# Optimization experiments

Measured on AMD Instinct MI355X. Metric: run time of the kernel, lower is better.

The kernel has to match this reference:

```python
import jax, jax.numpy as jnp
import numpy as np

N = 100000
E = 1000000
D = 32          # numerical_dim
HID = 64        # hidden_dim
OUT = 1         # output_dim
REL = 4 * D     # relation feature dim
EPS = 1e-8


def setup_inputs() -> dict:
    key = jax.random.key(0)
    k_x, k_e, k_w1, k_b1, k_w2, k_b2 = jax.random.split(key, 6)
    x = jax.random.uniform(k_x, (N, D), dtype=jnp.float32)
    edge_index = jax.random.randint(k_e, (2, E), 0, N, dtype=jnp.int64)
    # Linear params (PyTorch convention: W [out, in], y = x @ W.T + b)
    lim1 = 1.0 / np.sqrt(REL)
    W1 = jax.random.uniform(k_w1, (HID, REL), minval=-lim1, maxval=lim1, dtype=jnp.float32)
    b1 = jax.random.uniform(k_b1, (HID,), minval=-lim1, maxval=lim1, dtype=jnp.float32)
    lim2 = 1.0 / np.sqrt(HID)
    W2 = jax.random.uniform(k_w2, (OUT, HID), minval=-lim2, maxval=lim2, dtype=jnp.float32)
    b2 = jax.random.uniform(k_b2, (OUT,), minval=-lim2, maxval=lim2, dtype=jnp.float32)
    return {"x": x, "edge_index": edge_index, "W1": W1, "b1": b1, "W2": W2, "b2": b2}


def _relation_features(x_i, x_j):
    ratio = x_i / (x_j + EPS)
    log_ratio = jnp.log(x_i + EPS) - jnp.log(x_j + EPS)
    abs_diff = jnp.abs(x_i - x_j)
    rel_diff = abs_diff / (jnp.maximum(x_i, x_j) + EPS)
    return jnp.concatenate([ratio, log_ratio, abs_diff, rel_diff], axis=-1)  # [E, 4D]


def reference(x, edge_index, W1, b1, W2, b2):
    src, dst = edge_index[0], edge_index[1]
    x_i = x[src]                      # [E, D] gather source node feats
    x_j = x[dst]                      # [E, D] gather target node feats
    rel = _relation_features(x_i, x_j)  # [E, 4D]
    h = jax.nn.relu(rel @ W1.T + b1)    # [E, HID]
    edge_bias = (h @ W2.T + b2).squeeze(-1)  # [E]
    return edge_bias
```

## Files before the change

kernel.cpp:

```cpp
#include <hip/hip_runtime.h>


#define DD    32
#define HID   64
#define RELF  128
#define EPSF  1e-8f

typedef short  bf16x8 __attribute__((ext_vector_type(8)));
typedef float  f32x4  __attribute__((ext_vector_type(4)));

union U8 { unsigned u[4]; bf16x8 v; };

static __device__ __forceinline__ unsigned pk_tr(float lo, float hi) {
    return __builtin_amdgcn_perm(__builtin_bit_cast(unsigned, hi),
                                 __builtin_bit_cast(unsigned, lo), 0x07060302u);
}
static __device__ __forceinline__ unsigned rne_bits(float f) {
    unsigned u = __builtin_bit_cast(unsigned, f);
    return u + 0x7fffu + ((u >> 16) & 1u);
}
static __device__ __forceinline__ unsigned pk_rne(float lo, float hi) {
    return __builtin_amdgcn_perm(rne_bits(hi), rne_bits(lo), 0x07060302u);
}
static __device__ __forceinline__ float hi_f32(float f) {
    return __builtin_bit_cast(float, __builtin_bit_cast(unsigned, f) & 0xffff0000u);
}

__global__ __launch_bounds__(256)
void prep_logx(const float* __restrict__ x, unsigned* __restrict__ lx, int nq)
{
    int i = blockIdx.x * blockDim.x + threadIdx.x;
    if (i >= nq) return;
    float4 v = ((const float4*)x)[i];
    uint2 o;
    o.x = pk_rne(__logf(v.x + EPSF), __logf(v.y + EPSF));
    o.y = pk_rne(__logf(v.z + EPSF), __logf(v.w + EPSF));
    ((uint2*)lx)[i] = o;
}

template <int PRE>
__global__ __launch_bounds__(256, 2)
void edge_bias_mfma(const float* __restrict__ x,
                    const int*   __restrict__ ei,
                    const float* __restrict__ W1,
                    const float* __restrict__ b1,
                    const float* __restrict__ W2,
                    const float* __restrict__ b2,
                    const short* __restrict__ lx,
                    float* __restrict__ out,
                    int E)
{
    const int lane = threadIdx.x & 63;
    const int wave = (blockIdx.x * blockDim.x + threadIdx.x) >> 6;
    const int nwv  = (gridDim.x * blockDim.x) >> 6;
    const int c = lane & 15;
    const int q = lane >> 4;

    bf16x8 W0h[4], W0l[4], WL[4], WLn[4], WA[4], WDm[4];
    #pragma unroll
    for (int nt = 0; nt < 4; ++nt) {
        const float* wr = W1 + (nt * 16 + c) * RELF + q * 8;
        U8 h, l, t;
        #pragma unroll
        for (int p = 0; p < 4; ++p) {
            float w0 = wr[2 * p], w1 = wr[2 * p + 1];
            h.u[p] = pk_tr(w0, w1);
            l.u[p] = pk_rne(w0 - hi_f32(w0), w1 - hi_f32(w1));
        }
        W0h[nt] = h.v; W0l[nt] = l.v;
        #pragma unroll
        for (int p = 0; p < 4; ++p)
            t.u[p] = pk_rne(wr[32 + 2 * p], wr[32 + 2 * p + 1]);
        WL[nt] = t.v;
        #pragma unroll
        for (int p = 0; p < 4; ++p) t.u[p] ^= 0x80008000u;
        WLn[nt] = t.v;
        #pragma unroll
        for (int p = 0; p < 4; ++p)
            t.u[p] = pk_rne(wr[64 + 2 * p], wr[64 + 2 * p + 1]);
        WA[nt] = t.v;
        #pragma unroll
        for (int p = 0; p < 4; ++p)
            t.u[p] = pk_rne(wr[96 + 2 * p], wr[96 + 2 * p + 1]);
        WDm[nt] = t.v;
    }
    float b1v[4], w2v[4];
    #pragma unroll
    for (int nt = 0; nt < 4; ++nt) {
        b1v[nt] = b1[nt * 16 + c];
        w2v[nt] = W2[nt * 16 + c];
    }
    const float b2s = b2[0];

    const int ntiles = (E + 15) >> 4;
    for (int t = wave; t < ntiles; t += nwv) {
        const int e0 = t << 4;
        int em = e0 + c; if (em > E - 1) em = E - 1;
        const int src = ei[em];
        const int dst = ei[E + em];

        const float* pxi = x + (long)src * DD + q * 8;
        const float* pxj = x + (long)dst * DD + q * 8;
        float4 xi0 = ((const float4*)pxi)[0], xi1 = ((const float4*)pxi)[1];
        float4 xj0 = ((const float4*)pxj)[0], xj1 = ((const float4*)pxj)[1];
        float xiv[8] = {xi0.x, xi0.y, xi0.z, xi0.w, xi1.x, xi1.y, xi1.z, xi1.w};
        float xjv[8] = {xj0.x, xj0.y, xj0.z, xj0.w, xj1.x, xj1.y, xj1.z, xj1.w};

        bf16x8 aLi, aLj;
        if constexpr (PRE) {
            aLi = *(const bf16x8*)(lx + (long)src * DD + q * 8);
            aLj = *(const bf16x8*)(lx + (long)dst * DD + q * 8);
        } else {
            U8 ti, tj;
            #pragma unroll
            for (int p = 0; p < 4; ++p) {
                ti.u[p] = pk_rne(__logf(xiv[2*p] + EPSF), __logf(xiv[2*p+1] + EPSF));
                tj.u[p] = pk_rne(__logf(xjv[2*p] + EPSF), __logf(xjv[2*p+1] + EPSF));
            }
            aLi = ti.v; aLj = tj.v;
        }

        U8 R, Rl, Aa, Dd;
        #pragma unroll
        for (int p = 0; p < 4; ++p) {
            float a0 = xiv[2*p], a1 = xiv[2*p+1];
            float c0 = xjv[2*p], c1 = xjv[2*p+1];
            float r0 = a0 * __builtin_amdgcn_rcpf(c0 + EPSF);
            float r1 = a1 * __builtin_amdgcn_rcpf(c1 + EPSF);
            float d0 = fabsf(a0 - c0), d1 = fabsf(a1 - c1);
            float g0 = d0 * __builtin_amdgcn_rcpf(fmaxf(a0, c0) + EPSF);
            float g1 = d1 * __builtin_amdgcn_rcpf(fmaxf(a1, c1) + EPSF);
            R.u[p]  = pk_tr(r0, r1);
            Rl.u[p] = pk_tr(r0 - hi_f32(r0), r1 - hi_f32(r1));
            Aa.u[p] = pk_tr(d0, d1);
            Dd.u[p] = pk_tr(g0, g1);
        }

        f32x4 acc[4];
        #pragma unroll
        for (int nt = 0; nt < 4; ++nt) {
            acc[nt][0] = b1v[nt]; acc[nt][1] = b1v[nt];
            acc[nt][2] = b1v[nt]; acc[nt][3] = b1v[nt];
        }
        #pragma unroll
        for (int nt = 0; nt < 4; ++nt) {
            acc[nt] = __builtin_amdgcn_mfma_f32_16x16x32_bf16(R.v,  W0h[nt], acc[nt], 0, 0, 0);
            acc[nt] = __builtin_amdgcn_mfma_f32_16x16x32_bf16(Rl.v, W0h[nt], acc[nt], 0, 0, 0);
            acc[nt] = __builtin_amdgcn_mfma_f32_16x16x32_bf16(R.v,  W0l[nt], acc[nt], 0, 0, 0);
            acc[nt] = __builtin_amdgcn_mfma_f32_16x16x32_bf16(aLi,  WL[nt],  acc[nt], 0, 0, 0);
            acc[nt] = __builtin_amdgcn_mfma_f32_16x16x32_bf16(aLj,  WLn[nt], acc[nt], 0, 0, 0);
            acc[nt] = __builtin_amdgcn_mfma_f32_16x16x32_bf16(Aa.v, WA[nt],  acc[nt], 0, 0, 0);
            acc[nt] = __builtin_amdgcn_mfma_f32_16x16x32_bf16(Dd.v, WDm[nt], acc[nt], 0, 0, 0);
        }

        float p[4];
        #pragma unroll
        for (int r = 0; r < 4; ++r) {
            float pp = 0.f;
            #pragma unroll
            for (int nt = 0; nt < 4; ++nt)
                pp = fmaf(fmaxf(acc[nt][r], 0.f), w2v[nt], pp);
            pp += __shfl_xor(pp, 1);
            pp += __shfl_xor(pp, 2);
            pp += __shfl_xor(pp, 4);
            pp += __shfl_xor(pp, 8);
            p[r] = pp;
        }
        if (c < 4) {
            const int e = e0 + q * 4 + c;
            if (e < E) {
                float v = (c == 0) ? p[0] : (c == 1) ? p[1] : (c == 2) ? p[2] : p[3];
                out[e] = v + b2s;
            }
        }
    }
}

extern "C" void kernel_launch(void* const* d_in, const int* in_sizes, int n_in,
                              void* d_out, int out_size, void* d_ws, size_t ws_size,
                              hipStream_t stream)
{
    const float* x   = (const float*)d_in[0];
    const int*   ei  = (const int*)  d_in[1];
    const float* W1  = (const float*)d_in[2];
    const float* b1  = (const float*)d_in[3];
    const float* W2  = (const float*)d_in[4];
    const float* b2  = (const float*)d_in[5];
    float* out = (float*)d_out;

    const int E  = out_size;
    const int Nd = in_sizes[0];
    short* lx = (short*)d_ws;

    const bool pre = ws_size >= (size_t)Nd * sizeof(short) && (Nd % 4) == 0;
    if (pre) {
        const int nq = Nd / 4;
        prep_logx<<<(nq + 255) / 256, 256, 0, stream>>>(x, (unsigned*)lx, nq);
        edge_bias_mfma<1><<<1024, 256, 0, stream>>>(x, ei, W1, b1, W2, b2, lx, out, E);
    } else {
        edge_bias_mfma<0><<<1024, 256, 0, stream>>>(x, ei, W1, b1, W2, b2, lx, out, E);
    }
}
```

Measured before the change: 151.2 us.

## Software-pipeline edge index and feature gathers across tile iterations

Restructures the grid-stride loop so each wave prefetches the node features for the next tile and the edge indices for the tile after that while computing the current tile. This is meant to hide the dependent index-then-gather global memory latency behind the MFMA and elementwise work. In exchange it holds more live registers for the prefetched float4 and bf16x8 buffers, which can raise VGPR pressure under launch_bounds(256,2) and issue redundant loads on the final iterations.

```diff
diff --git a/kernel.cpp b/kernel.cpp
--- a/kernel.cpp
+++ b/kernel.cpp
@@ -60,7 +60,7 @@
     #pragma unroll
     for (int nt = 0; nt < 4; ++nt) {
         const float* wr = W1 + (nt * 16 + c) * RELF + q * 8;
-        U8 h, l, t;
+        U8 h, l, tt;
         #pragma unroll
         for (int p = 0; p < 4; ++p) {
             float w0 = wr[2 * p], w1 = wr[2 * p + 1];
@@ -70,19 +70,19 @@
         W0h[nt] = h.v; W0l[nt] = l.v;
         #pragma unroll
         for (int p = 0; p < 4; ++p)
-            t.u[p] = pk_rne(wr[32 + 2 * p], wr[32 + 2 * p + 1]);
-        WL[nt] = t.v;
-        #pragma unroll
-        for (int p = 0; p < 4; ++p) t.u[p] ^= 0x80008000u;
-        WLn[nt] = t.v;
+            tt.u[p] = pk_rne(wr[32 + 2 * p], wr[32 + 2 * p + 1]);
+        WL[nt] = tt.v;
+        #pragma unroll
+        for (int p = 0; p < 4; ++p) tt.u[p] ^= 0x80008000u;
+        WLn[nt] = tt.v;
         #pragma unroll
         for (int p = 0; p < 4; ++p)
-            t.u[p] = pk_rne(wr[64 + 2 * p], wr[64 + 2 * p + 1]);
-        WA[nt] = t.v;
+            tt.u[p] = pk_rne(wr[64 + 2 * p], wr[64 + 2 * p + 1]);
+        WA[nt] = tt.v;
         #pragma unroll
         for (int p = 0; p < 4; ++p)
-            t.u[p] = pk_rne(wr[96 + 2 * p], wr[96 + 2 * p + 1]);
-        WDm[nt] = t.v;
+            tt.u[p] = pk_rne(wr[96 + 2 * p], wr[96 + 2 * p + 1]);
+        WDm[nt] = tt.v;
     }
     float b1v[4], w2v[4];
     #pragma unroll
@@ -93,23 +93,58 @@
     const float b2s = b2[0];
 
     const int ntiles = (E + 15) >> 4;
-    for (int t = wave; t < ntiles; t += nwv) {
+    int t = wave;
+    if (t >= ntiles) return;
+
+    float4 xi0C, xi1C, xj0C, xj1C;
+    bf16x8 LiC, LjC;
+    int srcN, dstN;
+
+    {
+        int em = (t << 4) + c; if (em > E - 1) em = E - 1;
+        int s = ei[em], d = ei[E + em];
+        const float* pi = x + (long)s * DD + q * 8;
+        const float* pj = x + (long)d * DD + q * 8;
+        xi0C = ((const float4*)pi)[0]; xi1C = ((const float4*)pi)[1];
+        xj0C = ((const float4*)pj)[0]; xj1C = ((const float4*)pj)[1];
+        if (PRE) {
+            LiC = *(const bf16x8*)(lx + (long)s * DD + q * 8);
+            LjC = *(const bf16x8*)(lx + (long)d * DD + q * 8);
+        }
+    }
+    {
+        int t1 = t + nwv; if (t1 >= ntiles) t1 = t;
+        int em = (t1 << 4) + c; if (em > E - 1) em = E - 1;
+        srcN = ei[em]; dstN = ei[E + em];
+    }
+
+    for (; t < ntiles; t += nwv) {
+        float4 xi0N, xi1N, xj0N, xj1N;
+        bf16x8 LiN, LjN;
+        {
+            const float* pi = x + (long)srcN * DD + q * 8;
+            const float* pj = x + (long)dstN * DD + q * 8;
+            xi0N = ((const float4*)pi)[0]; xi1N = ((const float4*)pi)[1];
+            xj0N = ((const float4*)pj)[0]; xj1N = ((const float4*)pj)[1];
+            if (PRE) {
+                LiN = *(const bf16x8*)(lx + (long)srcN * DD + q * 8);
+                LjN = *(const bf16x8*)(lx + (long)dstN * DD + q * 8);
+            }
+        }
+        int srcN2, dstN2;
+        {
+            int t2 = t + 2 * nwv; if (t2 >= ntiles) t2 = t;
+            int em = (t2 << 4) + c; if (em > E - 1) em = E - 1;
+            srcN2 = ei[em]; dstN2 = ei[E + em];
+        }
+
         const int e0 = t << 4;
-        int em = e0 + c; if (em > E - 1) em = E - 1;
-        const int src = ei[em];
-        const int dst = ei[E + em];
-
-        const float* pxi = x + (long)src * DD + q * 8;
-        const float* pxj = x + (long)dst * DD + q * 8;
-        float4 xi0 = ((const float4*)pxi)[0], xi1 = ((const float4*)pxi)[1];
-        float4 xj0 = ((const float4*)pxj)[0], xj1 = ((const float4*)pxj)[1];
-        float xiv[8] = {xi0.x, xi0.y, xi0.z, xi0.w, xi1.x, xi1.y, xi1.z, xi1.w};
-        float xjv[8] = {xj0.x, xj0.y, xj0.z, xj0.w, xj1.x, xj1.y, xj1.z, xj1.w};
+        float xiv[8] = {xi0C.x, xi0C.y, xi0C.z, xi0C.w, xi1C.x, xi1C.y, xi1C.z, xi1C.w};
+        float xjv[8] = {xj0C.x, xj0C.y, xj0C.z, xj0C.w, xj1C.x, xj1C.y, xj1C.z, xj1C.w};
 
         bf16x8 aLi, aLj;
         if constexpr (PRE) {
-            aLi = *(const bf16x8*)(lx + (long)src * DD + q * 8);
-            aLj = *(const bf16x8*)(lx + (long)dst * DD + q * 8);
+            aLi = LiC; aLj = LjC;
         } else {
             U8 ti, tj;
             #pragma unroll
@@ -173,6 +208,10 @@
                 out[e] = v + b2s;
             }
         }
+
+        xi0C = xi0N; xi1C = xi1N; xj0C = xj0N; xj1C = xj1N;
+        LiC = LiN;  LjC = LjN;
+        srcN = srcN2; dstN = dstN2;
     }
 }
 
```

After: 144.9 us. -4.2%, faster.

## Software-pipeline edge index loads and feature gathers across tile iterations

Applied to the files above, without the earlier changes.

Restructures the persistent per-wave tile loop into a two-stage double-buffered pipeline. Node features and log features for the next tile are gathered, and edge indices two tiles ahead are loaded, while the current tile's MFMA work runs. The aim is to hide the dependent-index gather latency in a memory-bound kernel, at the cost of more live registers that may press on the 2-blocks-per-CU occupancy target. Out-of-range prefetch tiles are clamped to a valid tile so no loads go out of bounds.

```diff
diff --git a/kernel.cpp b/kernel.cpp
--- a/kernel.cpp
+++ b/kernel.cpp
@@ -60,7 +60,7 @@
     #pragma unroll
     for (int nt = 0; nt < 4; ++nt) {
         const float* wr = W1 + (nt * 16 + c) * RELF + q * 8;
-        U8 h, l, t;
+        U8 h, l, tt;
         #pragma unroll
         for (int p = 0; p < 4; ++p) {
             float w0 = wr[2 * p], w1 = wr[2 * p + 1];
@@ -70,19 +70,19 @@
         W0h[nt] = h.v; W0l[nt] = l.v;
         #pragma unroll
         for (int p = 0; p < 4; ++p)
-            t.u[p] = pk_rne(wr[32 + 2 * p], wr[32 + 2 * p + 1]);
-        WL[nt] = t.v;
-        #pragma unroll
-        for (int p = 0; p < 4; ++p) t.u[p] ^= 0x80008000u;
-        WLn[nt] = t.v;
+            tt.u[p] = pk_rne(wr[32 + 2 * p], wr[32 + 2 * p + 1]);
+        WL[nt] = tt.v;
+        #pragma unroll
+        for (int p = 0; p < 4; ++p) tt.u[p] ^= 0x80008000u;
+        WLn[nt] = tt.v;
         #pragma unroll
         for (int p = 0; p < 4; ++p)
-            t.u[p] = pk_rne(wr[64 + 2 * p], wr[64 + 2 * p + 1]);
-        WA[nt] = t.v;
+            tt.u[p] = pk_rne(wr[64 + 2 * p], wr[64 + 2 * p + 1]);
+        WA[nt] = tt.v;
         #pragma unroll
         for (int p = 0; p < 4; ++p)
-            t.u[p] = pk_rne(wr[96 + 2 * p], wr[96 + 2 * p + 1]);
-        WDm[nt] = t.v;
+            tt.u[p] = pk_rne(wr[96 + 2 * p], wr[96 + 2 * p + 1]);
+        WDm[nt] = tt.v;
     }
     float b1v[4], w2v[4];
     #pragma unroll
@@ -93,24 +93,33 @@
     const float b2s = b2[0];
 
     const int ntiles = (E + 15) >> 4;
-    for (int t = wave; t < ntiles; t += nwv) {
-        const int e0 = t << 4;
-        int em = e0 + c; if (em > E - 1) em = E - 1;
-        const int src = ei[em];
-        const int dst = ei[E + em];
-
-        const float* pxi = x + (long)src * DD + q * 8;
-        const float* pxj = x + (long)dst * DD + q * 8;
-        float4 xi0 = ((const float4*)pxi)[0], xi1 = ((const float4*)pxi)[1];
-        float4 xj0 = ((const float4*)pxj)[0], xj1 = ((const float4*)pxj)[1];
+    int t = wave;
+    if (t >= ntiles) return;
+
+    auto ldidx = [&](int tt, int& s, int& d) {
+        if (tt >= ntiles) tt = t;
+        int em = (tt << 4) + c; if (em > E - 1) em = E - 1;
+        s = ei[em]; d = ei[E + em];
+    };
+    auto gather = [&](int s, int d, float4& A0, float4& A1,
+                      float4& B0, float4& B1, bf16x8& Li, bf16x8& Lj) {
+        const float* pi = x + (long)s * DD + q * 8;
+        const float* pj = x + (long)d * DD + q * 8;
+        A0 = ((const float4*)pi)[0]; A1 = ((const float4*)pi)[1];
+        B0 = ((const float4*)pj)[0]; B1 = ((const float4*)pj)[1];
+        if constexpr (PRE) {
+            Li = *(const bf16x8*)(lx + (long)s * DD + q * 8);
+            Lj = *(const bf16x8*)(lx + (long)d * DD + q * 8);
+        } else { (void)Li; (void)Lj; }
+    };
+
+    auto compute = [&](int tc, float4 xi0, float4 xi1, float4 xj0, float4 xj1,
+                       bf16x8 aLi, bf16x8 aLj) {
+        const int e0 = tc << 4;
         float xiv[8] = {xi0.x, xi0.y, xi0.z, xi0.w, xi1.x, xi1.y, xi1.z, xi1.w};
         float xjv[8] = {xj0.x, xj0.y, xj0.z, xj0.w, xj1.x, xj1.y, xj1.z, xj1.w};
 
-        bf16x8 aLi, aLj;
-        if constexpr (PRE) {
-            aLi = *(const bf16x8*)(lx + (long)src * DD + q * 8);
-            aLj = *(const bf16x8*)(lx + (long)dst * DD + q * 8);
-        } else {
+        if constexpr (!PRE) {
             U8 ti, tj;
             #pragma unroll
             for (int p = 0; p < 4; ++p) {
@@ -173,6 +182,26 @@
                 out[e] = v + b2s;
             }
         }
+    };
+
+    float4 xA0, xA1, xA2, xA3; bf16x8 lA0, lA1;
+    float4 xB0, xB1, xB2, xB3; bf16x8 lB0, lB1;
+    int sC, dC;
+
+    { int s, d; ldidx(t,           s, d); gather(s, d, xA0, xA1, xA2, xA3, lA0, lA1); }
+    { int s, d; ldidx(t + nwv,     s, d); gather(s, d, xB0, xB1, xB2, xB3, lB0, lB1); }
+    ldidx(t + 2 * nwv, sC, dC);
+
+    for (;;) {
+        compute(t, xA0, xA1, xA2, xA3, lA0, lA1);
+        gather(sC, dC, xA0, xA1, xA2, xA3, lA0, lA1);
+        ldidx(t + 3 * nwv, sC, dC);
+        t += nwv; if (t >= ntiles) break;
+
+        compute(t, xB0, xB1, xB2, xB3, lB0, lB1);
+        gather(sC, dC, xB0, xB1, xB2, xB3, lB0, lB1);
+        ldidx(t + 3 * nwv, sC, dC);
+        t += nwv; if (t >= ntiles) break;
     }
 }
 
```

Result: faster. 147.6 us (-2.4%).
